# Kernel tuning notes

Hardware: AMD Instinct MI355X
Metric: run time of the kernel (lower is better)

## Reference

```python
import jax, jax.numpy as jnp
import numpy as np

A = 16          # n_agents
H = 128         # rnn_hidden_dim
IN = 128        # input_shape
NA = 32         # n_attention
NACT = 14       # n_actions
TAU = 0.5       # gumbel_softmax_tau
B_ENV = 1024    # parallel envs
BZ = B_ENV * A

# neighbor index: for agent i, all j != i (matches select_ind in torch code)
IDX = np.array([[j for j in range(A) if j != i] for i in range(A)])  # [A, A-1]


def gru_cell(x, h, Wih, Whh, bih, bhh):
    # torch GRUCell gate order: r, z, n
    gi = x @ Wih.T + bih
    gh = h @ Whh.T + bhh
    ir, iz, inn = jnp.split(gi, 3, axis=-1)
    hr, hz, hn = jnp.split(gh, 3, axis=-1)
    r = jax.nn.sigmoid(ir + hr)
    z = jax.nn.sigmoid(iz + hz)
    n = jnp.tanh(inn + r * hn)
    return (1.0 - z) * n + z * h


def run_gru(seq, Wih, Whh, bih, bhh):
    # seq: [T, N, D]; returns all hidden states [T, N, H]
    h0 = jnp.zeros((seq.shape[1], Whh.shape[1]), seq.dtype)
    def step(h, x):
        h2 = gru_cell(x, h, Wih, Whh, bih, bhh)
        return h2, h2
    _, ys = jax.lax.scan(step, h0, seq)
    return ys


def setup_inputs() -> dict:
    key = jax.random.key(0)
    ks = jax.random.split(key, 24)
    def u(k, shape, fan):
        s = 1.0 / np.sqrt(fan)
        return jax.random.uniform(k, shape, jnp.float32, -s, s)
    inp = {
        "inputs": jax.random.normal(ks[0], (BZ, IN), jnp.float32),
        "hidden_state": jax.random.normal(ks[1], (BZ, H), jnp.float32),
        "gumbel_u": jax.random.uniform(ks[2], (BZ * (A - 1), 2), jnp.float32),
        # fc1
        "W1": u(ks[3], (H, IN), IN), "b1": u(ks[4], (H,), IN),
        # GRUCell
        "Wih_c": u(ks[5], (3 * H, H), H), "Whh_c": u(ks[6], (3 * H, H), H),
        "bih_c": u(ks[7], (3 * H,), H), "bhh_c": u(ks[8], (3 * H,), H),
        # bi-GRU forward dir (input 2H)
        "Wih_f": u(ks[9], (3 * H, 2 * H), H), "Whh_f": u(ks[10], (3 * H, H), H),
        "bih_f": u(ks[11], (3 * H,), H), "bhh_f": u(ks[12], (3 * H,), H),
        # bi-GRU backward dir
        "Wih_b": u(ks[13], (3 * H, 2 * H), H), "Whh_b": u(ks[14], (3 * H, H), H),
        "bih_b": u(ks[15], (3 * H,), H), "bhh_b": u(ks[16], (3 * H,), H),
        # hard classifier
        "Wc": u(ks[17], (2, 2 * H), 2 * H), "bc": u(ks[18], (2,), 2 * H),
        # attention projections (no bias)
        "Wq": u(ks[19], (NA, H), H), "Wk": u(ks[20], (NA, H), H),
        # fc2
        "W2": u(ks[21], (NACT, 2 * H), 2 * H), "b2": u(ks[22], (NACT,), 2 * H),
    }
    return inp


def reference(inputs, hidden_state, gumbel_u, W1, b1, Wih_c, Whh_c, bih_c, bhh_c,
              Wih_f, Whh_f, bih_f, bhh_f, Wih_b, Whh_b, bih_b, bhh_b,
              Wc, bc, Wq, Wk, W2, b2):
    bz = inputs.shape[0]
    B = bz // A
    x1 = jax.nn.relu(inputs @ W1.T + b1)
    h_rnn = gru_cell(x1, hidden_state.reshape(-1, H), Wih_c, Whh_c, bih_c, bhh_c)  # [bz, H]

    h3 = h_rnn.reshape(B, A, H)
    nbr = h3[:, IDX, :]                                           # [B, A, A-1, H]
    self_rep = jnp.broadcast_to(h3[:, :, None, :], (B, A, A - 1, H))
    pairs = jnp.concatenate([self_rep, nbr], axis=-1)             # [B, A, A-1, 2H]
    seq = pairs.transpose(2, 0, 1, 3).reshape(A - 1, bz, 2 * H)   # [T, bz, 2H]

    yf = run_gru(seq, Wih_f, Whh_f, bih_f, bhh_f)
    yb = jnp.flip(run_gru(jnp.flip(seq, 0), Wih_b, Whh_b, bih_b, bhh_b), 0)
    h_hard = jnp.concatenate([yf, yb], axis=-1)                   # [T, bz, 2H]
    h_hard = h_hard.transpose(1, 0, 2).reshape(-1, 2 * H)         # [bz*T, 2H]

    logits = h_hard @ Wc.T + bc                                   # [bz*T, 2]
    g = -jnp.log(-jnp.log(gumbel_u + 1e-10) + 1e-10)
    gs = jax.nn.softmax((logits + g) / TAU, axis=-1)
    hard_w = gs[:, 1].reshape(B, A, A - 1)                        # hard gate

    q = (h_rnn @ Wq.T).reshape(B, A, NA)
    k = (h_rnn @ Wk.T).reshape(B, A, NA)
    kn = k[:, IDX, :] * hard_w[..., None]                         # [B, A, A-1, NA]
    scores = jnp.einsum('bad,bamd->bam', q, kn) / np.sqrt(NA)
    soft_w = jax.nn.softmax(scores, axis=-1)                      # [B, A, A-1]

    w = hard_w * soft_w
    agg = jnp.einsum('bam,bamh->bah', w, nbr).reshape(bz, H)
    out = jnp.concatenate([h_rnn, agg], axis=-1) @ W2.T + b2      # [bz, n_actions]
    return out, h_rnn
```

## Files before the change

kernel.cpp:

```cpp
#include <hip/hip_runtime.h>
#include <hip/hip_bf16.h>


typedef __attribute__((ext_vector_type(8))) short short8;
typedef __attribute__((ext_vector_type(4))) float float4v;

#define BF2F(x) __bfloat162float(x)
typedef __hip_bfloat16 bf;

__device__ __forceinline__ float frcp(float x) {
  return __builtin_amdgcn_rcpf(x);
}
__device__ __forceinline__ float fsigmoid(float x) {
  return frcp(1.f + __expf(-x));
}
__device__ __forceinline__ float ftanh(float x) {
  float e = __expf(2.f * x);
  return 1.f - 2.f * frcp(1.f + e);
}
__device__ __forceinline__ float rdv(const void* p, int i, int f) {
  return f ? ((const float*)p)[i] : BF2F(((const bf*)p)[i]);
}
__device__ __forceinline__ float upk(unsigned long long v, int s) {
  union { unsigned int i; float f; } x;
  x.i = ((unsigned int)((v >> s) & 0xffffULL)) << 16;
  return x.f;
}

static const int AO[23] = {
  0, 2097152, 4194304, 4685824, 4702208, 4702336, 4751488, 4800640, 4801024,
  4801408, 4899712, 4948864, 4949248, 4949632, 5047936, 5097088, 5097472,
  5097856, 5098368, 5098384, 5102480, 5106576, 5110160};
static const int AN[23] = {
  2097152, 2097152, 491520, 16384, 128, 49152, 49152, 384, 384, 98304, 49152,
  384, 384, 98304, 49152, 384, 384, 512, 2, 4096, 4096, 3584, 14};

struct CArgs {
  const void* src[23];
  int n[23];
  int off[23];
};

__global__ void kDetect(const unsigned short* __restrict__ p, int* flag) {
  __shared__ int s;
  if (threadIdx.x == 0) s = 0;
  __syncthreads();
  int hit = 0;
  for (int i = threadIdx.x; i < 4096; i += 1024) {
    int e = (p[i] >> 7) & 0xFF;
    if (e >= 0xC0) hit = 1;
  }
  if (hit) atomicOr(&s, 1);
  __syncthreads();
  if (threadIdx.x == 0) *flag = s;
}

__global__ void kConvert(CArgs a, const int* __restrict__ flag,
                         bf* __restrict__ arena) {
  const int b = blockIdx.y;
  const int n = a.n[b];
  const int f = *flag;
  bf* dst = arena + a.off[b];
  if (f) {
    const float* s = (const float*)a.src[b];
    for (int i = blockIdx.x * 256 + threadIdx.x; i < n; i += gridDim.x * 256)
      dst[i] = __float2bfloat16(s[i]);
  } else {
    const unsigned short* s = (const unsigned short*)a.src[b];
    unsigned short* d = (unsigned short*)dst;
    for (int i = blockIdx.x * 256 + threadIdx.x; i < n; i += gridDim.x * 256)
      d[i] = s[i];
  }
}

__global__ void kPrep(const bf* __restrict__ Wq, const bf* __restrict__ Wk,
                      const bf* __restrict__ W2a, const bf* __restrict__ WcA,
                      bf* __restrict__ Wqk, bf* __restrict__ W2p,
                      bf* __restrict__ Wcb) {
  int idx = blockIdx.x * 256 + threadIdx.x;
  if (idx < 8192) {
    int r = idx >> 7, c = idx & 127;
    Wqk[idx] = (r < 32) ? Wq[r * 128 + c] : Wk[(r - 32) * 128 + c];
  }
  if (idx < 4096)
    W2p[idx] = (idx < 3584) ? W2a[idx] : __float2bfloat16(0.f);
  if (idx < 512) {
    int dir = idx >> 8, l = (idx >> 7) & 1, k = idx & 127;
    Wcb[idx] = WcA[l * 256 + dir * 128 + k];
  }
}

__global__ __launch_bounds__(256) void kGemm(const bf* __restrict__ A,
                                             const bf* __restrict__ W,
                                             const bf* __restrict__ bias,
                                             bf* __restrict__ out,
                                             int N, int relu) {
  const int tid = threadIdx.x;
  const int wave = tid >> 6, lane = tid & 63;
  const int quad = lane >> 4, ci = lane & 15;
  const int mr = blockIdx.x * 64 + wave * 16;
  const int nbase = blockIdx.y * 64;
  const int ntiles = (N - nbase < 64) ? ((N - nbase) >> 4) : 4;

  float4v acc[4];
#pragma unroll
  for (int i = 0; i < 4; ++i) acc[i] = {0.f, 0.f, 0.f, 0.f};

#pragma unroll
  for (int ks = 0; ks < 4; ++ks) {
    short8 a = *(const short8*)(A + (size_t)(mr + ci) * 128 + ks * 32 + quad * 8);
    for (int nt = 0; nt < ntiles; ++nt) {
      short8 b = *(const short8*)(W + (size_t)(nbase + nt * 16 + ci) * 128 + ks * 32 + quad * 8);
      acc[nt] = __builtin_amdgcn_mfma_f32_16x16x32_bf16(a, b, acc[nt], 0, 0, 0);
    }
  }

  for (int nt = 0; nt < ntiles; ++nt) {
    int col = nbase + nt * 16 + ci;
    float bv = bias ? BF2F(bias[col]) : 0.f;
#pragma unroll
    for (int r = 0; r < 4; ++r) {
      int row = mr + quad * 4 + r;
      float v = acc[nt][r] + bv;
      if (relu) v = fmaxf(v, 0.f);
      out[(size_t)row * N + col] = __float2bfloat16(v);
    }
  }
}

__global__ __launch_bounds__(256, 4) void kStep(
    const bf* __restrict__ Hp, const bf* __restrict__ Whh,
    const bf* __restrict__ G, int gld,
    const bf* __restrict__ bhh,
    bf* __restrict__ Ho, float* __restrict__ HcopyF) {
  const int half = blockIdx.z;
  const int tid = threadIdx.x;
  const int wave = tid >> 6, lane = tid & 63;
  const int quad = lane >> 4, ci = lane & 15;
  const int mr = blockIdx.x * 64 + wave * 16;

  float4v acc[12];
#pragma unroll
  for (int i = 0; i < 12; ++i) acc[i] = {0.f, 0.f, 0.f, 0.f};

#pragma unroll
  for (int ks = 0; ks < 4; ++ks) {
    short8 a = *(const short8*)(Hp + (size_t)(mr + ci) * 128 + ks * 32 + quad * 8);
#pragma unroll
    for (int g = 0; g < 3; ++g)
#pragma unroll
      for (int nt = 0; nt < 4; ++nt) {
        short8 b = *(const short8*)(Whh + (size_t)(g * 128 + half * 64 + nt * 16 + ci) * 128 + ks * 32 + quad * 8);
        acc[g * 4 + nt] = __builtin_amdgcn_mfma_f32_16x16x32_bf16(a, b, acc[g * 4 + nt], 0, 0, 0);
      }
  }

  float bR[4], bZ[4], bN[4];
#pragma unroll
  for (int nt = 0; nt < 4; ++nt) {
    int c = half * 64 + nt * 16 + ci;
    bR[nt] = BF2F(bhh[c]);
    bZ[nt] = BF2F(bhh[128 + c]);
    bN[nt] = BF2F(bhh[256 + c]);
  }

#pragma unroll
  for (int r = 0; r < 4; ++r) {
    int rr = mr + quad * 4 + r;
    const bf* gs = G + (size_t)rr * gld;
#pragma unroll
    for (int nt = 0; nt < 4; ++nt) {
      int c = half * 64 + nt * 16 + ci;
      float gr = BF2F(gs[c]), gz = BF2F(gs[128 + c]), gnn = BF2F(gs[256 + c]);
      float pre_r = acc[nt][r] + gr + bR[nt];
      float pre_z = acc[4 + nt][r] + gz + bZ[nt];
      float hn_   = acc[8 + nt][r] + bN[nt];
      float rg = fsigmoid(pre_r);
      float zg = fsigmoid(pre_z);
      float ng = ftanh(gnn + rg * hn_);
      float hp = BF2F(Hp[(size_t)rr * 128 + c]);
      float hv = ng + zg * (hp - ng);
      Ho[(size_t)rr * 128 + c] = __float2bfloat16(hv);
      if (HcopyF) HcopyF[(size_t)rr * 128 + c] = hv;
    }
  }
}

__global__ __launch_bounds__(512, 4) void kSeq(
    const bf* __restrict__ hrnn,
    const bf* __restrict__ Wih_f, const bf* __restrict__ Wih_b,
    const bf* __restrict__ Whh_f, const bf* __restrict__ Whh_b,
    const bf* __restrict__ bih_f, const bf* __restrict__ bih_b,
    const bf* __restrict__ bhh_f, const bf* __restrict__ bhh_b,
    const bf* __restrict__ Wcb, float* __restrict__ L) {
  __shared__ unsigned long long sGiN[16][130];
  __shared__ bf sH[2][16][136];
  __shared__ float sL[16][15][2];
  __shared__ bf sWc[2][136];

  const int env = blockIdx.x;
  const int dir = blockIdx.y;
  const int tid = threadIdx.x;
  const int wave = tid >> 6, lane = tid & 63;
  const int nh = wave;
  const int quad = lane >> 4, ci = lane & 15;
  const bf* Wih = dir ? Wih_b : Wih_f;
  const bf* Whh = dir ? Whh_b : Whh_f;
  const bf* bih = dir ? bih_b : bih_f;
  const bf* bhh = dir ? bhh_b : bhh_f;
  const int cb = nh * 16 + ci;

  float4v gS[3], gN[3];
#pragma unroll
  for (int i = 0; i < 3; ++i) { gS[i] = {0.f, 0.f, 0.f, 0.f}; gN[i] = {0.f, 0.f, 0.f, 0.f}; }
#pragma unroll
  for (int ks = 0; ks < 4; ++ks) {
    short8 a = *(const short8*)(hrnn + (size_t)(env * 16 + ci) * 128 + ks * 32 + quad * 8);
#pragma unroll
    for (int g = 0; g < 3; ++g) {
      const bf* wrow = Wih + (size_t)(g * 128 + nh * 16 + ci) * 256 + ks * 32 + quad * 8;
      short8 bs = *(const short8*)(wrow);
      short8 bn = *(const short8*)(wrow + 128);
      gS[g] = __builtin_amdgcn_mfma_f32_16x16x32_bf16(a, bs, gS[g], 0, 0, 0);
      gN[g] = __builtin_amdgcn_mfma_f32_16x16x32_bf16(a, bn, gN[g], 0, 0, 0);
    }
  }
#pragma unroll
  for (int g = 0; g < 3; ++g) {
    int c = g * 128 + cb;
    float bv = BF2F(bih[c]);
    if (g < 2) bv += BF2F(bhh[c]);
#pragma unroll
    for (int r = 0; r < 4; ++r) gS[g][r] += bv;
  }
#pragma unroll
  for (int r = 0; r < 4; ++r) {
    unsigned long long pk = 0;
#pragma unroll
    for (int g = 0; g < 3; ++g) {
      bf b = __float2bfloat16(gN[g][r]);
      pk |= ((unsigned long long)(*(unsigned short*)&b)) << (16 * g);
    }
    sGiN[quad * 4 + r][cb] = pk;
  }

  {
    bf z = __float2bfloat16(0.f);
    bf* p = &sH[0][0][0];
    for (int i = tid; i < 16 * 136; i += 512) p[i] = z;
    if (tid < 256)
      sWc[tid >> 7][tid & 127] = Wcb[(dir * 2 + (tid >> 7)) * 128 + (tid & 127)];
  }

  short8 Bf[12];
#pragma unroll
  for (int g = 0; g < 3; ++g)
#pragma unroll
    for (int ks = 0; ks < 4; ++ks)
      Bf[g * 4 + ks] =
          *(const short8*)(Whh + (size_t)(g * 128 + nh * 16 + ci) * 128 + ks * 32 + quad * 8);

  float bNc = BF2F(bhh[256 + cb]);

  float hPrev[4];
#pragma unroll
  for (int r = 0; r < 4; ++r) hPrev[r] = 0.f;

  __syncthreads();

  for (int t = 0; t < 15; ++t) {
    const int cur = t & 1, nxt = cur ^ 1;
    const int m = dir ? (14 - t) : t;

    float4v acc[3];
#pragma unroll
    for (int i = 0; i < 3; ++i) acc[i] = {0.f, 0.f, 0.f, 0.f};
    float4v lacc = {0.f, 0.f, 0.f, 0.f};
#pragma unroll
    for (int ks = 0; ks < 4; ++ks) {
      short8 a = *(const short8*)&sH[cur][ci][ks * 32 + quad * 8];
#pragma unroll
      for (int g = 0; g < 3; ++g)
        acc[g] = __builtin_amdgcn_mfma_f32_16x16x32_bf16(a, Bf[g * 4 + ks], acc[g], 0, 0, 0);
      if (nh == 0) {
        short8 wv = *(const short8*)&sWc[ci & 1][ks * 32 + quad * 8];
        lacc = __builtin_amdgcn_mfma_f32_16x16x32_bf16(a, wv, lacc, 0, 0, 0);
      }
    }
    if (nh == 0 && t > 0 && ci < 2) {
      int mp = dir ? (15 - t) : (t - 1);
#pragma unroll
      for (int r = 0; r < 4; ++r) sL[quad * 4 + r][mp][ci] = lacc[r];
    }

#pragma unroll
    for (int r_ = 0; r_ < 4; ++r_) {
      int row = quad * 4 + r_;
      int jr = m + ((m >= row) ? 1 : 0);
      unsigned long long nb = sGiN[jr][cb];
      float pre_r = acc[0][r_] + gS[0][r_] + upk(nb, 0);
      float pre_z = acc[1][r_] + gS[1][r_] + upk(nb, 16);
      float gnn   = gS[2][r_] + upk(nb, 32);
      float hn_   = acc[2][r_] + bNc;
      float rg = fsigmoid(pre_r);
      float zg = fsigmoid(pre_z);
      float ng = ftanh(gnn + rg * hn_);
      float hp = hPrev[r_];
      float hv = ng + zg * (hp - ng);
      hPrev[r_] = hv;
      sH[nxt][row][cb] = __float2bfloat16(hv);
    }
    __syncthreads();
  }

  if (nh == 0) {
    float4v lacc = {0.f, 0.f, 0.f, 0.f};
#pragma unroll
    for (int ks = 0; ks < 4; ++ks) {
      short8 a = *(const short8*)&sH[1][ci][ks * 32 + quad * 8];
      short8 wv = *(const short8*)&sWc[ci & 1][ks * 32 + quad * 8];
      lacc = __builtin_amdgcn_mfma_f32_16x16x32_bf16(a, wv, lacc, 0, 0, 0);
    }
    if (ci < 2) {
      int mf = dir ? 0 : 14;
#pragma unroll
      for (int r = 0; r < 4; ++r) sL[quad * 4 + r][mf][ci] = lacc[r];
    }
  }
  __syncthreads();

  for (int i = tid; i < 480; i += 512) {
    int row = i / 30, rem = i - row * 30;
    int mm = rem >> 1, l = rem & 1;
    L[(size_t)((env * 16 + row) * 15 + mm) * 4 + dir * 2 + l] = sL[row][mm][l];
  }
}

__global__ void kGumbel(const float* __restrict__ L, const void* __restrict__ guRaw,
                        const int* __restrict__ flag, const void* __restrict__ bcRaw,
                        float* __restrict__ hw) {
  int idx = blockIdx.x * 256 + threadIdx.x;
  if (idx >= 245760) return;
  const int f = *flag;
  const float* Lp = L + (size_t)idx * 4;
  float l0 = Lp[0] + Lp[2] + rdv(bcRaw, 0, f);
  float l1 = Lp[1] + Lp[3] + rdv(bcRaw, 1, f);
  float u0 = rdv(guRaw, idx * 2, f);
  float u1 = rdv(guRaw, idx * 2 + 1, f);
  float g0 = -__logf(-__logf(u0 + 1e-10f) + 1e-10f);
  float g1 = -__logf(-__logf(u1 + 1e-10f) + 1e-10f);
  float d = ((l1 + g1) - (l0 + g0)) * 2.0f;
  hw[idx] = fsigmoid(d);
}

__global__ __launch_bounds__(256) void kAttn(
    const bf* __restrict__ h, const bf* __restrict__ qk,
    const float* __restrict__ hw, bf* __restrict__ aggB) {
  __shared__ float sh[16 * 132];
  __shared__ float sqk[16 * 64];
  __shared__ float shw[16 * 15];
  __shared__ float sw[16 * 16];
  int bb = blockIdx.x, tid = threadIdx.x;

  for (int i = tid; i < 2048; i += 256)
    sh[(i >> 7) * 132 + (i & 127)] = BF2F(h[(size_t)bb * 2048 + i]);
  for (int i = tid; i < 1024; i += 256)
    sqk[i] = BF2F(qk[(size_t)bb * 1024 + i]);
  for (int i = tid; i < 240; i += 256) shw[i] = hw[bb * 240 + i];
  __syncthreads();

  int a = tid >> 4, i = tid & 15;
  float s = -1e30f;
  if (i < 15) {
    int j = i + (i >= a);
    float d = 0.f;
#pragma unroll
    for (int c = 0; c < 32; ++c) d += sqk[a * 64 + c] * sqk[j * 64 + 32 + c];
    s = shw[a * 15 + i] * d * 0.17677669529663687f;
  }
  float mx = s;
#pragma unroll
  for (int d = 1; d < 16; d <<= 1) mx = fmaxf(mx, __shfl_xor(mx, d));
  float e = (i < 15) ? __expf(s - mx) : 0.f;
  float sum = e;
#pragma unroll
  for (int d = 1; d < 16; d <<= 1) sum += __shfl_xor(sum, d);
  float w = (i < 15) ? (e * frcp(sum)) * shw[a * 15 + i] : 0.f;
  sw[a * 16 + i] = w;
  __syncthreads();

  float ac[8] = {0, 0, 0, 0, 0, 0, 0, 0};
  for (int mm = 0; mm < 15; ++mm) {
    int jm = mm + (mm >= a);
    float wm = sw[a * 16 + mm];
    const float* shp = &sh[jm * 132 + i * 8];
    float4 h0 = *(const float4*)shp;
    float4 h1 = *(const float4*)(shp + 4);
    ac[0] += wm * h0.x; ac[1] += wm * h0.y; ac[2] += wm * h0.z; ac[3] += wm * h0.w;
    ac[4] += wm * h1.x; ac[5] += wm * h1.y; ac[6] += wm * h1.z; ac[7] += wm * h1.w;
  }
  short8 v;
#pragma unroll
  for (int d = 0; d < 8; ++d) {
    bf b = __float2bfloat16(ac[d]);
    v[d] = *(short*)&b;
  }
  *(short8*)(aggB + (size_t)(bb * 16 + a) * 128 + i * 8) = v;
}

__global__ __launch_bounds__(256) void kGemmOut(
    const bf* __restrict__ hrnn, const bf* __restrict__ aggB,
    const bf* __restrict__ W2p, const void* __restrict__ b2Raw,
    const int* __restrict__ flag, float* __restrict__ out) {
  const int tid = threadIdx.x;
  const int wave = tid >> 6, lane = tid & 63;
  const int quad = lane >> 4, ci = lane & 15;
  const int mr = blockIdx.x * 64 + wave * 16;
  const int f = *flag;

  float4v acc = {0.f, 0.f, 0.f, 0.f};
#pragma unroll
  for (int ks = 0; ks < 8; ++ks) {
    const bf* src = (ks < 4) ? hrnn : aggB;
    int k = (ks & 3) * 32 + quad * 8;
    short8 a = *(const short8*)(src + (size_t)(mr + ci) * 128 + k);
    short8 b = *(const short8*)(W2p + (size_t)ci * 256 + ks * 32 + quad * 8);
    acc = __builtin_amdgcn_mfma_f32_16x16x32_bf16(a, b, acc, 0, 0, 0);
  }

  if (ci < 14) {
    float bv = rdv(b2Raw, ci, f);
#pragma unroll
    for (int r = 0; r < 4; ++r)
      out[(size_t)(mr + quad * 4 + r) * 14 + ci] = acc[r] + bv;
  }
}

extern "C" void kernel_launch(void* const* d_in, const int* in_sizes, int n_in,
                              void* d_out, int out_size, void* d_ws, size_t ws_size,
                              hipStream_t stream) {
  const size_t OFF_ARENA = 0;
  const size_t OFF_FLAG  = 10220544;
  const size_t OFF_A     = 10220800;
  const size_t OFF_WQK   = 26998016;
  const size_t OFF_WCB   = 27014400;
  const size_t OFF_W2P   = 27410944;
  const size_t OFF_HRNN  = 27419136;
  const size_t OFF_QK    = 31613440;
  const size_t NEEDED    = 84042240;
  if (ws_size < NEEDED) return;
  if (n_in < 23 || in_sizes[0] != 2097152 || in_sizes[3] != 16384 ||
      in_sizes[5] != 49152 || in_sizes[9] != 98304 || in_sizes[17] != 512 ||
      in_sizes[19] != 4096 || in_sizes[21] != 3584 || out_size != 2326528)
    return;

  char* ws = (char*)d_ws;
  bf*    arena = (bf*)(ws + OFF_ARENA);
  float* L     = (float*)(ws + OFF_ARENA);
  int*   flag  = (int*)(ws + OFF_FLAG);
  bf*    x1    = (bf*)(ws + OFF_A);
  bf*    gi_c  = (bf*)(ws + OFF_A + 4194304);
  float* hw    = (float*)(ws + OFF_A);
  bf*    aggB  = (bf*)(ws + OFF_A + 983040);
  bf*    Wqk   = (bf*)(ws + OFF_WQK);
  bf*    Wcb   = (bf*)(ws + OFF_WCB);
  bf*    W2p   = (bf*)(ws + OFF_W2P);
  bf*    hrnn  = (bf*)(ws + OFF_HRNN);
  bf*    qk    = (bf*)(ws + OFF_QK);

  float* out14 = (float*)d_out;
  float* outh  = (float*)d_out + 229376;

  kDetect<<<1, 1024, 0, stream>>>((const unsigned short*)d_in[0], flag);
  CArgs ca;
  for (int i = 0; i < 23; ++i) { ca.src[i] = d_in[i]; ca.n[i] = AN[i]; ca.off[i] = AO[i]; }
  kConvert<<<dim3(128, 23), 256, 0, stream>>>(ca, flag, arena);

  const bf* inputs = arena + AO[0];
  const bf* hidden = arena + AO[1];
  const bf* W1     = arena + AO[3];
  const bf* b1     = arena + AO[4];
  const bf* Wih_c  = arena + AO[5];
  const bf* Whh_c  = arena + AO[6];
  const bf* bih_c  = arena + AO[7];
  const bf* bhh_c  = arena + AO[8];
  const bf* Wih_f  = arena + AO[9];
  const bf* Whh_f  = arena + AO[10];
  const bf* bih_f  = arena + AO[11];
  const bf* bhh_f  = arena + AO[12];
  const bf* Wih_b  = arena + AO[13];
  const bf* Whh_b  = arena + AO[14];
  const bf* bih_b  = arena + AO[15];
  const bf* bhh_b  = arena + AO[16];
  const bf* WcA    = arena + AO[17];
  const bf* Wq     = arena + AO[19];
  const bf* Wk     = arena + AO[20];
  const bf* W2a    = arena + AO[21];

  kPrep<<<dim3(32), 256, 0, stream>>>(Wq, Wk, W2a, WcA, Wqk, W2p, Wcb);
  kGemm<<<dim3(256, 2), 256, 0, stream>>>(inputs, W1, b1, x1, 128, 1);
  kGemm<<<dim3(256, 6), 256, 0, stream>>>(x1, Wih_c, bih_c, gi_c, 384, 0);
  kStep<<<dim3(256, 1, 2), 256, 0, stream>>>(hidden, Whh_c, gi_c, 384, bhh_c,
                                             hrnn, outh);
  kGemm<<<dim3(256, 1), 256, 0, stream>>>(hrnn, Wqk, (const bf*)nullptr, qk, 64, 0);

  kSeq<<<dim3(1024, 2), 512, 0, stream>>>(hrnn, Wih_f, Wih_b, Whh_f, Whh_b,
                                          bih_f, bih_b, bhh_f, bhh_b, Wcb, L);

  kGumbel<<<dim3(960), 256, 0, stream>>>(L, d_in[2], flag, d_in[18], hw);
  kAttn<<<dim3(1024), 256, 0, stream>>>(hrnn, qk, hw, aggB);
  kGemmOut<<<dim3(256), 256, 0, stream>>>(hrnn, aggB, W2p, d_in[22], flag, out14);
}
```

Baseline: 311.9 us.

## Fuse prep, QK projection and gumbel into neighbors; vectorize convert and GRU stores

Folds the weight-prep kernel into the convert kernel, skips converting inputs that are read raw elsewhere, and vectorizes the fp32-to-bf16 conversion. The Q/K projection GEMM and the Gumbel gate kernel are fused into the attention kernel, removing two launches and their intermediate global round trips. In the bidirectional GRU kernel the MFMA operands are swapped so each lane owns four consecutive hidden columns, which allows vector LDS loads of the gate inputs and packed 4-element hidden-state stores. The trade-off is that each attention block recomputes its small Q/K projection itself.

```diff
diff --git a/kernel.cpp b/kernel.cpp
--- a/kernel.cpp
+++ b/kernel.cpp
@@ -3,7 +3,9 @@
 
 
 typedef __attribute__((ext_vector_type(8))) short short8;
+typedef __attribute__((ext_vector_type(4))) short short4v;
 typedef __attribute__((ext_vector_type(4))) float float4v;
+typedef __attribute__((ext_vector_type(2))) unsigned long long ull2;
 
 #define BF2F(x) __bfloat162float(x)
 typedef __hip_bfloat16 bf;
@@ -56,37 +58,59 @@
 }
 
 __global__ void kConvert(CArgs a, const int* __restrict__ flag,
-                         bf* __restrict__ arena) {
+                         bf* __restrict__ arena,
+                         const void* __restrict__ WqR, const void* __restrict__ WkR,
+                         const void* __restrict__ W2R, const void* __restrict__ WcR,
+                         bf* __restrict__ Wqk, bf* __restrict__ W2p,
+                         bf* __restrict__ Wcb) {
   const int b = blockIdx.y;
+  const int f = *flag;
+  if (b == 23) {
+    int idx = blockIdx.x * 256 + threadIdx.x;
+    if (idx < 8192) {
+      int r = idx >> 7, c = idx & 127;
+      float v = (r < 32) ? rdv(WqR, r * 128 + c, f) : rdv(WkR, (r - 32) * 128 + c, f);
+      Wqk[idx] = __float2bfloat16(v);
+    }
+    if (idx < 4096)
+      W2p[idx] = __float2bfloat16((idx < 3584) ? rdv(W2R, idx, f) : 0.f);
+    if (idx < 512) {
+      int dir = idx >> 8, l = (idx >> 7) & 1, k = idx & 127;
+      Wcb[idx] = __float2bfloat16(rdv(WcR, l * 256 + dir * 128 + k, f));
+    }
+    return;
+  }
+  if (b == 2 || b == 18 || b == 22) return;
   const int n = a.n[b];
-  const int f = *flag;
+  const int nv = n & ~7;
   bf* dst = arena + a.off[b];
+  const int gid = blockIdx.x * 256 + threadIdx.x;
+  const int gs = gridDim.x * 256;
   if (f) {
     const float* s = (const float*)a.src[b];
-    for (int i = blockIdx.x * 256 + threadIdx.x; i < n; i += gridDim.x * 256)
-      dst[i] = __float2bfloat16(s[i]);
+    for (int i = gid * 8; i < nv; i += gs * 8) {
+      float4 x0 = *(const float4*)(s + i);
+      float4 x1 = *(const float4*)(s + i + 4);
+      short8 v;
+      bf t;
+      t = __float2bfloat16(x0.x); v[0] = *(short*)&t;
+      t = __float2bfloat16(x0.y); v[1] = *(short*)&t;
+      t = __float2bfloat16(x0.z); v[2] = *(short*)&t;
+      t = __float2bfloat16(x0.w); v[3] = *(short*)&t;
+      t = __float2bfloat16(x1.x); v[4] = *(short*)&t;
+      t = __float2bfloat16(x1.y); v[5] = *(short*)&t;
+      t = __float2bfloat16(x1.z); v[6] = *(short*)&t;
+      t = __float2bfloat16(x1.w); v[7] = *(short*)&t;
+      *(short8*)(dst + i) = v;
+    }
+    for (int i = nv + gid; i < n; i += gs) dst[i] = __float2bfloat16(s[i]);
   } else {
-    const unsigned short* s = (const unsigned short*)a.src[b];
-    unsigned short* d = (unsigned short*)dst;
-    for (int i = blockIdx.x * 256 + threadIdx.x; i < n; i += gridDim.x * 256)
-      d[i] = s[i];
-  }
-}
-
-__global__ void kPrep(const bf* __restrict__ Wq, const bf* __restrict__ Wk,
-                      const bf* __restrict__ W2a, const bf* __restrict__ WcA,
-                      bf* __restrict__ Wqk, bf* __restrict__ W2p,
-                      bf* __restrict__ Wcb) {
-  int idx = blockIdx.x * 256 + threadIdx.x;
-  if (idx < 8192) {
-    int r = idx >> 7, c = idx & 127;
-    Wqk[idx] = (r < 32) ? Wq[r * 128 + c] : Wk[(r - 32) * 128 + c];
-  }
-  if (idx < 4096)
-    W2p[idx] = (idx < 3584) ? W2a[idx] : __float2bfloat16(0.f);
-  if (idx < 512) {
-    int dir = idx >> 8, l = (idx >> 7) & 1, k = idx & 127;
-    Wcb[idx] = WcA[l * 256 + dir * 128 + k];
+    const short8* s = (const short8*)a.src[b];
+    short8* d = (short8*)dst;
+    for (int i = gid; i * 8 < nv; i += gs) d[i] = s[i];
+    const unsigned short* ss = (const unsigned short*)a.src[b];
+    unsigned short* ds = (unsigned short*)dst;
+    for (int i = nv + gid; i < n; i += gs) ds[i] = ss[i];
   }
 }
 
@@ -208,31 +232,32 @@
   const bf* Whh = dir ? Whh_b : Whh_f;
   const bf* bih = dir ? bih_b : bih_f;
   const bf* bhh = dir ? bhh_b : bhh_f;
-  const int cb = nh * 16 + ci;
+  const int h0q = nh * 16 + quad * 4;
 
   float4v gS[3], gN[3];
 #pragma unroll
   for (int i = 0; i < 3; ++i) { gS[i] = {0.f, 0.f, 0.f, 0.f}; gN[i] = {0.f, 0.f, 0.f, 0.f}; }
 #pragma unroll
   for (int ks = 0; ks < 4; ++ks) {
-    short8 a = *(const short8*)(hrnn + (size_t)(env * 16 + ci) * 128 + ks * 32 + quad * 8);
+    short8 bh = *(const short8*)(hrnn + (size_t)(env * 16 + ci) * 128 + ks * 32 + quad * 8);
 #pragma unroll
     for (int g = 0; g < 3; ++g) {
       const bf* wrow = Wih + (size_t)(g * 128 + nh * 16 + ci) * 256 + ks * 32 + quad * 8;
-      short8 bs = *(const short8*)(wrow);
-      short8 bn = *(const short8*)(wrow + 128);
-      gS[g] = __builtin_amdgcn_mfma_f32_16x16x32_bf16(a, bs, gS[g], 0, 0, 0);
-      gN[g] = __builtin_amdgcn_mfma_f32_16x16x32_bf16(a, bn, gN[g], 0, 0, 0);
-    }
-  }
-#pragma unroll
-  for (int g = 0; g < 3; ++g) {
-    int c = g * 128 + cb;
-    float bv = BF2F(bih[c]);
-    if (g < 2) bv += BF2F(bhh[c]);
-#pragma unroll
-    for (int r = 0; r < 4; ++r) gS[g][r] += bv;
-  }
+      short8 ws = *(const short8*)(wrow);
+      short8 wn = *(const short8*)(wrow + 128);
+      gS[g] = __builtin_amdgcn_mfma_f32_16x16x32_bf16(ws, bh, gS[g], 0, 0, 0);
+      gN[g] = __builtin_amdgcn_mfma_f32_16x16x32_bf16(wn, bh, gN[g], 0, 0, 0);
+    }
+  }
+#pragma unroll
+  for (int g = 0; g < 3; ++g)
+#pragma unroll
+    for (int r = 0; r < 4; ++r) {
+      int c = g * 128 + h0q + r;
+      float bv = BF2F(bih[c]);
+      if (g < 2) bv += BF2F(bhh[c]);
+      gS[g][r] += bv;
+    }
 #pragma unroll
   for (int r = 0; r < 4; ++r) {
     unsigned long long pk = 0;
@@ -241,7 +266,7 @@
       bf b = __float2bfloat16(gN[g][r]);
       pk |= ((unsigned long long)(*(unsigned short*)&b)) << (16 * g);
     }
-    sGiN[quad * 4 + r][cb] = pk;
+    sGiN[ci][h0q + r] = pk;
   }
 
   {
@@ -260,7 +285,9 @@
       Bf[g * 4 + ks] =
           *(const short8*)(Whh + (size_t)(g * 128 + nh * 16 + ci) * 128 + ks * 32 + quad * 8);
 
-  float bNc = BF2F(bhh[256 + cb]);
+  float bNc[4];
+#pragma unroll
+  for (int r = 0; r < 4; ++r) bNc[r] = BF2F(bhh[256 + h0q + r]);
 
   float hPrev[4];
 #pragma unroll
@@ -271,6 +298,10 @@
   for (int t = 0; t < 15; ++t) {
     const int cur = t & 1, nxt = cur ^ 1;
     const int m = dir ? (14 - t) : t;
+    const int jr = m + ((m >= ci) ? 1 : 0);
+
+    ull2 nb01 = *(const ull2*)&sGiN[jr][h0q];
+    ull2 nb23 = *(const ull2*)&sGiN[jr][h0q + 2];
 
     float4v acc[3];
 #pragma unroll
@@ -278,38 +309,39 @@
     float4v lacc = {0.f, 0.f, 0.f, 0.f};
 #pragma unroll
     for (int ks = 0; ks < 4; ++ks) {
-      short8 a = *(const short8*)&sH[cur][ci][ks * 32 + quad * 8];
+      short8 bh = *(const short8*)&sH[cur][ci][ks * 32 + quad * 8];
 #pragma unroll
       for (int g = 0; g < 3; ++g)
-        acc[g] = __builtin_amdgcn_mfma_f32_16x16x32_bf16(a, Bf[g * 4 + ks], acc[g], 0, 0, 0);
+        acc[g] = __builtin_amdgcn_mfma_f32_16x16x32_bf16(Bf[g * 4 + ks], bh, acc[g], 0, 0, 0);
       if (nh == 0) {
         short8 wv = *(const short8*)&sWc[ci & 1][ks * 32 + quad * 8];
-        lacc = __builtin_amdgcn_mfma_f32_16x16x32_bf16(a, wv, lacc, 0, 0, 0);
+        lacc = __builtin_amdgcn_mfma_f32_16x16x32_bf16(wv, bh, lacc, 0, 0, 0);
       }
     }
-    if (nh == 0 && t > 0 && ci < 2) {
+    if (nh == 0 && t > 0 && quad == 0) {
       int mp = dir ? (15 - t) : (t - 1);
-#pragma unroll
-      for (int r = 0; r < 4; ++r) sL[quad * 4 + r][mp][ci] = lacc[r];
-    }
-
-#pragma unroll
-    for (int r_ = 0; r_ < 4; ++r_) {
-      int row = quad * 4 + r_;
-      int jr = m + ((m >= row) ? 1 : 0);
-      unsigned long long nb = sGiN[jr][cb];
-      float pre_r = acc[0][r_] + gS[0][r_] + upk(nb, 0);
-      float pre_z = acc[1][r_] + gS[1][r_] + upk(nb, 16);
-      float gnn   = gS[2][r_] + upk(nb, 32);
-      float hn_   = acc[2][r_] + bNc;
+      sL[ci][mp][0] = lacc[0];
+      sL[ci][mp][1] = lacc[1];
+    }
+
+    short4v hv4;
+#pragma unroll
+    for (int r = 0; r < 4; ++r) {
+      unsigned long long nb = (r == 0) ? nb01.x : (r == 1) ? nb01.y
+                             : (r == 2) ? nb23.x : nb23.y;
+      float pre_r = acc[0][r] + gS[0][r] + upk(nb, 0);
+      float pre_z = acc[1][r] + gS[1][r] + upk(nb, 16);
+      float gnn   = gS[2][r] + upk(nb, 32);
+      float hn_   = acc[2][r] + bNc[r];
       float rg = fsigmoid(pre_r);
       float zg = fsigmoid(pre_z);
       float ng = ftanh(gnn + rg * hn_);
-      float hp = hPrev[r_];
-      float hv = ng + zg * (hp - ng);
-      hPrev[r_] = hv;
-      sH[nxt][row][cb] = __float2bfloat16(hv);
-    }
+      float hv = ng + zg * (hPrev[r] - ng);
+      hPrev[r] = hv;
+      bf b = __float2bfloat16(hv);
+      hv4[r] = *(short*)&b;
+    }
+    *(short4v*)&sH[nxt][ci][h0q] = hv4;
     __syncthreads();
   }
 
@@ -317,14 +349,14 @@
     float4v lacc = {0.f, 0.f, 0.f, 0.f};
 #pragma unroll
     for (int ks = 0; ks < 4; ++ks) {
-      short8 a = *(const short8*)&sH[1][ci][ks * 32 + quad * 8];
+      short8 bh = *(const short8*)&sH[1][ci][ks * 32 + quad * 8];
       short8 wv = *(const short8*)&sWc[ci & 1][ks * 32 + quad * 8];
-      lacc = __builtin_amdgcn_mfma_f32_16x16x32_bf16(a, wv, lacc, 0, 0, 0);
-    }
-    if (ci < 2) {
+      lacc = __builtin_amdgcn_mfma_f32_16x16x32_bf16(wv, bh, lacc, 0, 0, 0);
+    }
+    if (quad == 0) {
       int mf = dir ? 0 : 14;
-#pragma unroll
-      for (int r = 0; r < 4; ++r) sL[quad * 4 + r][mf][ci] = lacc[r];
+      sL[ci][mf][0] = lacc[0];
+      sL[ci][mf][1] = lacc[1];
     }
   }
   __syncthreads();
@@ -336,37 +368,45 @@
   }
 }
 
-__global__ void kGumbel(const float* __restrict__ L, const void* __restrict__ guRaw,
-                        const int* __restrict__ flag, const void* __restrict__ bcRaw,
-                        float* __restrict__ hw) {
-  int idx = blockIdx.x * 256 + threadIdx.x;
-  if (idx >= 245760) return;
-  const int f = *flag;
-  const float* Lp = L + (size_t)idx * 4;
-  float l0 = Lp[0] + Lp[2] + rdv(bcRaw, 0, f);
-  float l1 = Lp[1] + Lp[3] + rdv(bcRaw, 1, f);
-  float u0 = rdv(guRaw, idx * 2, f);
-  float u1 = rdv(guRaw, idx * 2 + 1, f);
-  float g0 = -__logf(-__logf(u0 + 1e-10f) + 1e-10f);
-  float g1 = -__logf(-__logf(u1 + 1e-10f) + 1e-10f);
-  float d = ((l1 + g1) - (l0 + g0)) * 2.0f;
-  hw[idx] = fsigmoid(d);
-}
-
 __global__ __launch_bounds__(256) void kAttn(
-    const bf* __restrict__ h, const bf* __restrict__ qk,
-    const float* __restrict__ hw, bf* __restrict__ aggB) {
+    const bf* __restrict__ h, const bf* __restrict__ Wqk,
+    const float* __restrict__ L, const void* __restrict__ guRaw,
+    const void* __restrict__ bcRaw, const int* __restrict__ flag,
+    bf* __restrict__ aggB) {
   __shared__ float sh[16 * 132];
   __shared__ float sqk[16 * 64];
   __shared__ float shw[16 * 15];
   __shared__ float sw[16 * 16];
   int bb = blockIdx.x, tid = threadIdx.x;
-
+  const int f = *flag;
+
+  {
+    const int w = tid >> 6, lane = tid & 63;
+    const int quad = lane >> 4, ci = lane & 15;
+    float4v acc = {0.f, 0.f, 0.f, 0.f};
+#pragma unroll
+    for (int ks = 0; ks < 4; ++ks) {
+      short8 a_ = *(const short8*)(h + (size_t)(bb * 16 + ci) * 128 + ks * 32 + quad * 8);
+      short8 b_ = *(const short8*)(Wqk + (size_t)(w * 16 + ci) * 128 + ks * 32 + quad * 8);
+      acc = __builtin_amdgcn_mfma_f32_16x16x32_bf16(a_, b_, acc, 0, 0, 0);
+    }
+#pragma unroll
+    for (int r = 0; r < 4; ++r)
+      sqk[(quad * 4 + r) * 64 + w * 16 + ci] = acc[r];
+  }
   for (int i = tid; i < 2048; i += 256)
     sh[(i >> 7) * 132 + (i & 127)] = BF2F(h[(size_t)bb * 2048 + i]);
-  for (int i = tid; i < 1024; i += 256)
-    sqk[i] = BF2F(qk[(size_t)bb * 1024 + i]);
-  for (int i = tid; i < 240; i += 256) shw[i] = hw[bb * 240 + i];
+  if (tid < 240) {
+    int idx = bb * 240 + tid;
+    const float* Lp = L + (size_t)idx * 4;
+    float l0 = Lp[0] + Lp[2] + rdv(bcRaw, 0, f);
+    float l1 = Lp[1] + Lp[3] + rdv(bcRaw, 1, f);
+    float u0 = rdv(guRaw, idx * 2, f);
+    float u1 = rdv(guRaw, idx * 2 + 1, f);
+    float g0 = -__logf(-__logf(u0 + 1e-10f) + 1e-10f);
+    float g1 = -__logf(-__logf(u1 + 1e-10f) + 1e-10f);
+    shw[tid] = fsigmoid(((l1 + g1) - (l0 + g0)) * 2.0f);
+  }
   __syncthreads();
 
   int a = tid >> 4, i = tid & 15;
@@ -446,7 +486,6 @@
   const size_t OFF_WCB   = 27014400;
   const size_t OFF_W2P   = 27410944;
   const size_t OFF_HRNN  = 27419136;
-  const size_t OFF_QK    = 31613440;
   const size_t NEEDED    = 84042240;
   if (ws_size < NEEDED) return;
   if (n_in < 23 || in_sizes[0] != 2097152 || in_sizes[3] != 16384 ||
@@ -460,13 +499,11 @@
   int*   flag  = (int*)(ws + OFF_FLAG);
   bf*    x1    = (bf*)(ws + OFF_A);
   bf*    gi_c  = (bf*)(ws + OFF_A + 4194304);
-  float* hw    = (float*)(ws + OFF_A);
   bf*    aggB  = (bf*)(ws + OFF_A + 983040);
   bf*    Wqk   = (bf*)(ws + OFF_WQK);
   bf*    Wcb   = (bf*)(ws + OFF_WCB);
   bf*    W2p   = (bf*)(ws + OFF_W2P);
   bf*    hrnn  = (bf*)(ws + OFF_HRNN);
-  bf*    qk    = (bf*)(ws + OFF_QK);
 
   float* out14 = (float*)d_out;
   float* outh  = (float*)d_out + 229376;
@@ -474,7 +511,9 @@
   kDetect<<<1, 1024, 0, stream>>>((const unsigned short*)d_in[0], flag);
   CArgs ca;
   for (int i = 0; i < 23; ++i) { ca.src[i] = d_in[i]; ca.n[i] = AN[i]; ca.off[i] = AO[i]; }
-  kConvert<<<dim3(128, 23), 256, 0, stream>>>(ca, flag, arena);
+  kConvert<<<dim3(128, 24), 256, 0, stream>>>(ca, flag, arena,
+                                              d_in[19], d_in[20], d_in[21], d_in[17],
+                                              Wqk, W2p, Wcb);
 
   const bf* inputs = arena + AO[0];
   const bf* hidden = arena + AO[1];
@@ -492,22 +531,16 @@
   const bf* Whh_b  = arena + AO[14];
   const bf* bih_b  = arena + AO[15];
   const bf* bhh_b  = arena + AO[16];
-  const bf* WcA    = arena + AO[17];
-  const bf* Wq     = arena + AO[19];
-  const bf* Wk     = arena + AO[20];
-  const bf* W2a    = arena + AO[21];
-
-  kPrep<<<dim3(32), 256, 0, stream>>>(Wq, Wk, W2a, WcA, Wqk, W2p, Wcb);
+
   kGemm<<<dim3(256, 2), 256, 0, stream>>>(inputs, W1, b1, x1, 128, 1);
   kGemm<<<dim3(256, 6), 256, 0, stream>>>(x1, Wih_c, bih_c, gi_c, 384, 0);
   kStep<<<dim3(256, 1, 2), 256, 0, stream>>>(hidden, Whh_c, gi_c, 384, bhh_c,
                                              hrnn, outh);
-  kGemm<<<dim3(256, 1), 256, 0, stream>>>(hrnn, Wqk, (const bf*)nullptr, qk, 64, 0);
 
   kSeq<<<dim3(1024, 2), 512, 0, stream>>>(hrnn, Wih_f, Wih_b, Whh_f, Whh_b,
                                           bih_f, bih_b, bhh_f, bhh_b, Wcb, L);
 
-  kGumbel<<<dim3(960), 256, 0, stream>>>(L, d_in[2], flag, d_in[18], hw);
-  kAttn<<<dim3(1024), 256, 0, stream>>>(hrnn, qk, hw, aggB);
+  kAttn<<<dim3(1024), 256, 0, stream>>>(hrnn, Wqk, L, d_in[2], d_in[18], flag,
+                                        aggB);
   kGemmOut<<<dim3(256), 256, 0, stream>>>(hrnn, aggB, W2p, d_in[22], flag, out14);
 }
```

Result: faster. 280.5 us (-10.1%).
